# Optimization experiments

Hardware: AMD Instinct MI355X
Metric: run time of the kernel (lower is better)

Reference implementation:

```python
import jax, jax.numpy as jnp
import numpy as np

ENV_NUM = 4
# test_env = ['env1'] -> train envs are {0, 2, 3}; train pair indices i*4+j for i,j in {0,2,3}
TRAIN_INDEX = np.array([0, 2, 3, 8, 10, 11, 12, 14, 15])
CHUNK = 8  # grid points processed per step (original batch_len=4)


def setup_inputs() -> dict:
    key = jax.random.key(0)
    k1, k2 = jax.random.split(key)
    E, L, S, F = 4, 10, 1024, 256
    matrix = jax.random.normal(k1, (E, L, S, F), dtype=jnp.float32)
    # number of valid (non-padded) samples per (env, label); rest are zero-padded
    data_len = jax.random.randint(k2, (E, L), S // 2, S + 1).astype(jnp.float32)
    params = jnp.eye(F, dtype=jnp.float32)  # module initializes params = eye(feature_num)
    return {"matrix": matrix, "data_len": data_len, "params": params, "sample_size": 1024}


def _kde_forward(matrix, data_len, params, sample_size):
    E, L, S, F = matrix.shape
    bw = float(S) ** (-1.0 / 5.0)                 # max_sample ** (-1/(1+4))
    c = -0.5 / (bw * bw)                          # offset ** z == exp(c * z)
    divisor = np.sqrt(2.0 * np.pi) * bw

    m = jnp.einsum('elsf,fg->elsg', matrix, params)   # (E,L,S,F)
    # torch uses .item() for min/max -> constants w.r.t. autodiff
    left = jax.lax.stop_gradient(jnp.min(m))
    right = jax.lax.stop_gradient(jnp.max(m))
    delta = (right - left) / sample_size
    x_grid = jnp.linspace(left, right, sample_size)   # (sample_size,)

    S_f = jnp.float32(S)
    dl3 = data_len[:, :, None]                        # (E,L,1)

    def body(acc, pts):                               # pts: (CHUNK,)
        # Gaussian kernel values, (E,L,S,F,CHUNK) -- the big streamed intermediate
        z = jnp.exp(c * jnp.square(m[..., None] - pts))
        ksum = jnp.sum(z, axis=2)                     # (E,L,F,CHUNK)
        # remove contribution of the (S - data_len) zero-padded samples
        zero_corr = ((S_f - dl3) * jnp.exp(c * jnp.square(pts)))[:, :, None, :]  # (E,L,1,CHUNK)
        red = (ksum - zero_corr) / dl3[..., None]     # (E,L,F,CHUNK)
        # sum_p |red_i - red_j| over grid chunk -> (E,E,L,F)
        acc = acc + jnp.sum(jnp.abs(red[None, :] - red[:, None]), axis=-1)
        return acc, None

    n_chunks = sample_size // CHUNK
    init = jnp.zeros((E, E, L, F), dtype=matrix.dtype)
    store, _ = jax.lax.scan(body, init, x_grid.reshape(n_chunks, CHUNK))
    store_dis = store.reshape(E * E, L, F) / divisor  # divisor is constant per step

    scaled = store_dis * (delta / 2.0)
    test_results = jnp.max(scaled, axis=0)                      # (L,F)
    train_results = jnp.max(scaled[TRAIN_INDEX], axis=0)        # (L,F)
    return train_results, test_results


def reference(matrix, data_len, params, sample_size):
    return _kde_forward(matrix, data_len, params, sample_size)
```

## Files before the change

### kernel.cpp

```cpp
#include <hip/hip_runtime.h>
#include <hip/hip_fp16.h>
#include <math.h>

#define E_ 4
#define L_ 10
#define S_ 1024
#define F_ 256
#define T_ 1024
#define NROW (E_*L_*S_)
#define NBLK (NROW/64)
#define NH   48
#define CSW  224

#define OFF_PMIN 64
#define OFF_PMAX 2048
#define OFF_M   32768
#define OFF_CS  (32768 + (size_t)NROW * F_)
#define OFF_BT  (OFF_CS + (size_t)40 * F_ * CSW / 2)
#define OFF_PT  (OFF_BT + (size_t)T_ * CSW / 2)

typedef _Float16 half8 __attribute__((ext_vector_type(8)));
typedef __fp16 h2v __attribute__((ext_vector_type(2)));
typedef float f32x4v __attribute__((ext_vector_type(4)));

__device__ __forceinline__ void put_hl(_Float16* p, float v) {
  _Float16 h = (_Float16)v;
  _Float16 l = (_Float16)(v - (float)h);
  p[0] = h; p[1] = l;
}

__device__ __forceinline__ void stpk(_Float16* b, int row, int lane,
                                     float x, float y) {
  const int hi = row * 128 + ((2 * lane) ^ ((row & 7) << 3));
  *(h2v*)(b + hi) = __builtin_amdgcn_cvt_pkrtz(x, y);
}
__device__ __forceinline__ void stpk_rne(_Float16* b, int row, int lane,
                                         float x, float y) {
  const int hi = row * 128 + ((2 * lane) ^ ((row & 7) << 3));
  h2v v;
  v[0] = (__fp16)x;
  v[1] = (__fp16)y;
  *(h2v*)(b + hi) = v;
}

__global__ __launch_bounds__(256) void k_pt(const float* __restrict__ P,
                                            _Float16* __restrict__ PT) {
  const int k = blockIdx.x;
  const int c = threadIdx.x;
  PT[(size_t)c * F_ + k] = (_Float16)P[(size_t)k * F_ + c];
}

__global__ __launch_bounds__(256) void k0_mfma(const float* __restrict__ A,
                                               const _Float16* __restrict__ PT,
                                               float* __restrict__ MT,
                                               float* __restrict__ pmin,
                                               float* __restrict__ pmax) {
  __shared__ __align__(16) _Float16 Ahi[64][40];
  __shared__ __align__(16) _Float16 Alo[64][40];
  __shared__ __align__(16) _Float16 Bl[256][40];
  __shared__ float wmin[4], wmax[4];
  const int tid = threadIdx.x;
  const int wave = tid >> 6, lane = tid & 63;
  const int nn = lane & 15, quad = lane >> 4;
  const int row0 = blockIdx.x * 64;
  const int el = blockIdx.x >> 4;
  const int s0 = (blockIdx.x & 15) * 64;
  const int r = tid >> 2, part = tid & 3;
  const float* asrc = A + (size_t)(row0 + r) * F_ + part * 8;
  const _Float16* bbase = PT + (size_t)tid * F_;
  f32x4v acc[4][4];
#pragma unroll
  for (int rt = 0; rt < 4; ++rt)
#pragma unroll
    for (int ct = 0; ct < 4; ++ct) acc[rt][ct] = (f32x4v){0.f, 0.f, 0.f, 0.f};

  float4 pa0 = ((const float4*)asrc)[0];
  float4 pa1 = ((const float4*)asrc)[1];
  int4 pb0, pb1, pb2, pb3;
  {
    const int4* bs = (const int4*)bbase;
    pb0 = bs[0]; pb1 = bs[1]; pb2 = bs[2]; pb3 = bs[3];
  }

  for (int kc = 0; kc < 8; ++kc) {
    __syncthreads();
    {
      float vv[8] = {pa0.x, pa0.y, pa0.z, pa0.w, pa1.x, pa1.y, pa1.z, pa1.w};
      half8 hh, hl;
#pragma unroll
      for (int j = 0; j < 8; ++j) {
        _Float16 h = (_Float16)vv[j];
        hh[j] = h;
        hl[j] = (_Float16)(vv[j] - (float)h);
      }
      *(half8*)&Ahi[r][part * 8] = hh;
      *(half8*)&Alo[r][part * 8] = hl;
      int4* bd = (int4*)&Bl[tid][0];
      bd[0] = pb0; bd[1] = pb1; bd[2] = pb2; bd[3] = pb3;
    }
    if (kc < 7) {
      const float* an = asrc + (kc + 1) * 32;
      pa0 = ((const float4*)an)[0];
      pa1 = ((const float4*)an)[1];
      const int4* bn = (const int4*)(bbase + (kc + 1) * 32);
      pb0 = bn[0]; pb1 = bn[1]; pb2 = bn[2]; pb3 = bn[3];
    }
    __syncthreads();
    half8 afh[4], afl[4], bf[4];
#pragma unroll
    for (int rt = 0; rt < 4; ++rt) {
      afh[rt] = *(const half8*)&Ahi[rt * 16 + nn][quad * 8];
      afl[rt] = *(const half8*)&Alo[rt * 16 + nn][quad * 8];
    }
#pragma unroll
    for (int ct = 0; ct < 4; ++ct)
      bf[ct] = *(const half8*)&Bl[wave * 64 + ct * 16 + nn][quad * 8];
#pragma unroll
    for (int rt = 0; rt < 4; ++rt)
#pragma unroll
      for (int ct = 0; ct < 4; ++ct) {
        acc[rt][ct] = __builtin_amdgcn_mfma_f32_16x16x32_f16(afh[rt], bf[ct], acc[rt][ct], 0, 0, 0);
        acc[rt][ct] = __builtin_amdgcn_mfma_f32_16x16x32_f16(afl[rt], bf[ct], acc[rt][ct], 0, 0, 0);
      }
  }
  float vmin = 3.4e38f, vmax = -3.4e38f;
#pragma unroll
  for (int rt = 0; rt < 4; ++rt)
#pragma unroll
    for (int ct = 0; ct < 4; ++ct) {
      f32x4v c = acc[rt][ct];
      const int col = wave * 64 + ct * 16 + nn;
      const int sl = s0 + rt * 16 + quad * 4;
      *(float4*)&MT[((size_t)el * F_ + col) * S_ + sl] =
          make_float4(c[0], c[1], c[2], c[3]);
      vmin = fminf(vmin, fminf(fminf(c[0], c[1]), fminf(c[2], c[3])));
      vmax = fmaxf(vmax, fmaxf(fmaxf(c[0], c[1]), fmaxf(c[2], c[3])));
    }
#pragma unroll
  for (int off = 32; off; off >>= 1) {
    vmin = fminf(vmin, __shfl_down(vmin, off));
    vmax = fmaxf(vmax, __shfl_down(vmax, off));
  }
  if (lane == 0) { wmin[wave] = vmin; wmax[wave] = vmax; }
  __syncthreads();
  if (tid == 0) {
    pmin[blockIdx.x] = fminf(fminf(wmin[0], wmin[1]), fminf(wmin[2], wmin[3]));
    pmax[blockIdx.x] = fmaxf(fmaxf(wmax[0], wmax[1]), fmaxf(wmax[2], wmax[3]));
  }
}

__global__ __launch_bounds__(256) void k1_setup(const float* __restrict__ pmin,
                                                const float* __restrict__ pmax,
                                                float* __restrict__ hdr) {
  __shared__ float sm[4], sx[4];
  const int tid = threadIdx.x;
  float vmin = 3.4e38f, vmax = -3.4e38f;
  for (int i = tid; i < NBLK; i += 256) {
    vmin = fminf(vmin, pmin[i]);
    vmax = fmaxf(vmax, pmax[i]);
  }
#pragma unroll
  for (int off = 32; off; off >>= 1) {
    vmin = fminf(vmin, __shfl_down(vmin, off));
    vmax = fmaxf(vmax, __shfl_down(vmax, off));
  }
  if ((tid & 63) == 0) { sm[tid >> 6] = vmin; sx[tid >> 6] = vmax; }
  __syncthreads();
  if (tid == 0) {
    const float left = fminf(fminf(sm[0], sm[1]), fminf(sm[2], sm[3]));
    const float right = fmaxf(fmaxf(sx[0], sx[1]), fmaxf(sx[2], sx[3]));
    const float dg = (right - left) / 1023.0f;
    const float delta = (right - left) / 1024.0f;
    const float divisor = 0.62665706865775006f;
    const float scale = delta * 0.5f / divisor;
    const float Pp = (right - left) + 5.0f;
    const float sqpi8 = 0.62665706865775006f;
    hdr[0] = left; hdr[1] = dg; hdr[2] = 0.f; hdr[3] = scale;
    hdr[4] = 6.2831853071795864f / Pp;
    hdr[5] = 2.0f * sqpi8 / Pp;
    hdr[6] = sqpi8 / Pp;
  }
}

__global__ __launch_bounds__(256) void kB(const float* __restrict__ hdr,
                                          _Float16* __restrict__ BT) {
  const int t = blockIdx.x;
  const int j = threadIdx.x;
  if (j >= CSW) return;
  const float left = hdr[0], dg = hdr[1];
  const float w1 = hdr[4], asc = hdr[5], a0 = hdr[6];
  const float x = left + (float)t * dg;
  float v = 0.f;
  const int kidx = j >> 1;
  if (j < 2 * (2 * NH + 1)) {
    if (kidx == 0) v = a0;
    else if (kidx <= NH) {
      float wk = w1 * (float)kidx;
      v = asc * expf(-wk * wk * 0.03125f) * __cosf(wk * x);
    } else {
      float wk = w1 * (float)(kidx - NH);
      v = asc * expf(-wk * wk * 0.03125f) * __sinf(wk * x);
    }
  }
  BT[(size_t)t * CSW + j] = (_Float16)v;
}

__global__ __launch_bounds__(64) void kF(const float* __restrict__ MT,
                                         const float* __restrict__ hdr,
                                         _Float16* __restrict__ CS) {
  __shared__ __align__(16) _Float16 Ah[16 * 128];
  __shared__ __align__(16) _Float16 Bh[16 * 128];
  const int lane = threadIdx.x;
  const int el = blockIdx.x >> 8;
  const int f = blockIdx.x & 255;
  const float w1 = hdr[4];
  const float* src = MT + ((size_t)el * F_ + f) * S_;
  _Float16* csrow = CS + ((size_t)el * F_ + f) * CSW;

  stpk(Ah, 0, lane, 1.f, 1.f);
  stpk(Ah, 1, lane, 0.f, 0.f);
  stpk(Ah, 14, lane, 0.f, 0.f);
  stpk(Ah, 15, lane, 0.f, 0.f);
  stpk(Bh, 0, lane, 1.f, 1.f);
  stpk(Bh, 1, lane, 0.f, 0.f);

  f32x4v acc = (f32x4v){0.f, 0.f, 0.f, 0.f};
  const int rw = lane & 15, quad = lane >> 4;

  float2 nxt = ((const float2*)src)[lane];
  for (int bt = 0; bt < 8; ++bt) {
    float2 cur = nxt;
    if (bt < 7) nxt = ((const float2*)src)[(bt + 1) * 64 + lane];
    float aa = w1 * cur.x, ab = w1 * cur.y;
    float s1a, c1a, s1b, c1b;
    __sincosf(aa, &s1a, &c1a);
    __sincosf(ab, &s1b, &c1b);
    const float tca = c1a + c1a, tcb = c1b + c1b;
    stpk_rne(Bh, 2, lane, c1a, c1b);
    stpk_rne(Bh, 3, lane, s1a, s1b);
    float cpa = c1a, cppa = 1.f, spa = s1a, sppa = 0.f;
    float cpb = c1b, cppb = 1.f, spb = s1b, sppb = 0.f;
    float c2a = 0.f, c2b = 0.f, s2a = 0.f, s2b = 0.f;
#pragma unroll
    for (int rr = 2; rr <= 7; ++rr) {
      float cna = fmaf(tca, cpa, -cppa);
      float cnb = fmaf(tcb, cpb, -cppb);
      float sna = fmaf(tca, spa, -sppa);
      float snb = fmaf(tcb, spb, -sppb);
      if (rr == 2) { c2a = cna; c2b = cnb; s2a = sna; s2b = snb; }
      stpk_rne(Bh, 2 * rr, lane, cna, cnb);
      stpk_rne(Bh, 2 * rr + 1, lane, sna, snb);
      cppa = cpa; cpa = cna; cppb = cpb; cpb = cnb;
      sppa = spa; spa = sna; sppb = spb; spb = snb;
    }
    float d2a = c2a + c2a, d2b = c2b + c2b;
    float c4a = fmaf(d2a, c2a, -1.f), c4b = fmaf(d2b, c2b, -1.f);
    float s4a = d2a * s2a, s4b = d2b * s2b;
    float d4a = c4a + c4a, d4b = c4b + c4b;
    float c8a = fmaf(d4a, c4a, -1.f), c8b = fmaf(d4b, c4b, -1.f);
    float s8a = d4a * s4a, s8b = d4b * s4b;
    stpk_rne(Ah, 2, lane, c8a, c8b);
    stpk_rne(Ah, 3, lane, s8a, s8b);
    const float tqa = c8a + c8a, tqb = c8b + c8b;
    float qca = c8a, qcpa = 1.f, qsa = s8a, qspa = 0.f;
    float qcb = c8b, qcpb = 1.f, qsb = s8b, qspb = 0.f;
#pragma unroll
    for (int q = 2; q <= 6; ++q) {
      float cna = fmaf(tqa, qca, -qcpa);
      float cnb = fmaf(tqb, qcb, -qcpb);
      float sna = fmaf(tqa, qsa, -qspa);
      float snb = fmaf(tqb, qsb, -qspb);
      stpk_rne(Ah, 2 * q, lane, cna, cnb);
      stpk_rne(Ah, 2 * q + 1, lane, sna, snb);
      qcpa = qca; qca = cna; qcpb = qcb; qcb = cnb;
      qspa = qsa; qsa = sna; qspb = qsb; qsb = snb;
    }
#pragma unroll
    for (int kc = 0; kc < 4; ++kc) {
      const int off = rw * 128 + ((kc * 32 + quad * 8) ^ ((rw & 7) << 3));
      half8 af = *(const half8*)(Ah + off);
      half8 bhf = *(const half8*)(Bh + off);
      acc = __builtin_amdgcn_mfma_f32_16x16x32_f16(af, bhf, acc, 0, 0, 0);
    }
  }
  float a0 = acc[0], a1 = acc[1], a2 = acc[2], a3 = acc[3];
  float p0 = __shfl_xor(a0, 1), p1 = __shfl_xor(a1, 1);
  float p2 = __shfl_xor(a2, 1), p3 = __shfl_xor(a3, 1);
  if ((rw & 1) == 0) {
    const int rr = rw >> 1;
    const int k0v = 16 * quad + rr;
    const int k1v = 16 * quad + 8 + rr;
    float C0 = a0 - p1, S0 = a1 + p0;
    float C1 = a2 - p3, S1 = a3 + p2;
    if (k0v == 0) {
      csrow[0] = (_Float16)1024.f;
      csrow[1] = (_Float16)0.f;
    }
    if (k0v >= 1 && k0v <= NH) {
      put_hl(csrow + 2 * k0v, C0);
      put_hl(csrow + 2 * (NH + k0v), S0);
    }
    if (k1v <= NH) {
      put_hl(csrow + 2 * k1v, C1);
      put_hl(csrow + 2 * (NH + k1v), S1);
    }
  }
  if (lane < 15) {
    h2v z;
    z[0] = (__fp16)0.f;
    z[1] = (__fp16)0.f;
    *(h2v*)(csrow + 194 + 2 * lane) = z;
  }
}

__global__ __launch_bounds__(256) void kR(const _Float16* __restrict__ CS,
                                          const _Float16* __restrict__ BT,
                                          float* __restrict__ OUT) {
  const int tid = threadIdx.x;
  const int wave = tid >> 6, lane = tid & 63;
  const int nn = lane & 15, quad = lane >> 4;
  const int el = blockIdx.x >> 4;
  const int t0 = (blockIdx.x & 15) << 6;

  const _Float16* ab0 = CS + ((size_t)el * F_ + wave * 64 + 0 * 16 + nn) * CSW + quad * 8;
  const _Float16* ab1 = CS + ((size_t)el * F_ + wave * 64 + 1 * 16 + nn) * CSW + quad * 8;
  const _Float16* ab2 = CS + ((size_t)el * F_ + wave * 64 + 2 * 16 + nn) * CSW + quad * 8;
  const _Float16* ab3 = CS + ((size_t)el * F_ + wave * 64 + 3 * 16 + nn) * CSW + quad * 8;
  const _Float16* bb0 = BT + (size_t)(t0 + 0 * 16 + nn) * CSW + quad * 8;
  const _Float16* bb1 = BT + (size_t)(t0 + 1 * 16 + nn) * CSW + quad * 8;
  const _Float16* bb2 = BT + (size_t)(t0 + 2 * 16 + nn) * CSW + quad * 8;
  const _Float16* bb3 = BT + (size_t)(t0 + 3 * 16 + nn) * CSW + quad * 8;

  f32x4v acc[4][4];
#pragma unroll
  for (int ft = 0; ft < 4; ++ft)
#pragma unroll
    for (int tn = 0; tn < 4; ++tn) acc[ft][tn] = (f32x4v){0.f, 0.f, 0.f, 0.f};

  half8 pa[4], pb[4];
  pa[0] = *(const half8*)ab0; pa[1] = *(const half8*)ab1;
  pa[2] = *(const half8*)ab2; pa[3] = *(const half8*)ab3;
  pb[0] = *(const half8*)bb0; pb[1] = *(const half8*)bb1;
  pb[2] = *(const half8*)bb2; pb[3] = *(const half8*)bb3;

#pragma unroll
  for (int kc = 0; kc < CSW / 32; ++kc) {
    half8 af[4], bf[4];
#pragma unroll
    for (int ft = 0; ft < 4; ++ft) af[ft] = pa[ft];
#pragma unroll
    for (int tn = 0; tn < 4; ++tn) bf[tn] = pb[tn];
    if (kc < CSW / 32 - 1) {
      const int o = (kc + 1) * 32;
      pa[0] = *(const half8*)(ab0 + o); pa[1] = *(const half8*)(ab1 + o);
      pa[2] = *(const half8*)(ab2 + o); pa[3] = *(const half8*)(ab3 + o);
      pb[0] = *(const half8*)(bb0 + o); pb[1] = *(const half8*)(bb1 + o);
      pb[2] = *(const half8*)(bb2 + o); pb[3] = *(const half8*)(bb3 + o);
    }
#pragma unroll
    for (int ft = 0; ft < 4; ++ft)
#pragma unroll
      for (int tn = 0; tn < 4; ++tn)
        acc[ft][tn] = __builtin_amdgcn_mfma_f32_16x16x32_f16(af[ft], bf[tn], acc[ft][tn], 0, 0, 0);
  }

  float* Ob = OUT + (size_t)el * F_ * T_ + t0;
#pragma unroll
  for (int ft = 0; ft < 4; ++ft)
#pragma unroll
    for (int tn = 0; tn < 4; ++tn) {
      f32x4v c = acc[ft][tn];
      const int fb = wave * 64 + ft * 16 + quad * 4;
      const int tc = tn * 16 + nn;
      Ob[(size_t)(fb + 0) * T_ + tc] = c[0];
      Ob[(size_t)(fb + 1) * T_ + tc] = c[1];
      Ob[(size_t)(fb + 2) * T_ + tc] = c[2];
      Ob[(size_t)(fb + 3) * T_ + tc] = c[3];
    }
}

__global__ __launch_bounds__(256) void k4_epi(const float* __restrict__ OUT,
                                              const float* __restrict__ hdr,
                                              const float* __restrict__ dl,
                                              float* __restrict__ out) {
  __shared__ float rs[4][6];
  const int tid = threadIdx.x;
  const int l = blockIdx.x >> 8;
  const int f = blockIdx.x & 255;
  const float left = hdr[0], dg = hdr[1], scale = hdr[3];
  const int t = 4 * tid;
  float etv[4];
#pragma unroll
  for (int d = 0; d < 4; ++d) {
    float x = left + (float)(t + d) * dg;
    etv[d] = expf(-8.0f * x * x);
  }
  float red[E_][4];
#pragma unroll
  for (int e = 0; e < E_; ++e) {
    float4 ks = *(const float4*)(OUT + (((size_t)(e * L_ + l)) * F_ + f) * T_ + t);
    const float dlv = dl[e * L_ + l];
    const float zc = (float)S_ - dlv;
    const float idl = 1.0f / dlv;
    red[e][0] = (ks.x - zc * etv[0]) * idl;
    red[e][1] = (ks.y - zc * etv[1]) * idl;
    red[e][2] = (ks.z - zc * etv[2]) * idl;
    red[e][3] = (ks.w - zc * etv[3]) * idl;
  }
  float D[6];
  const int pa[6] = {0, 0, 0, 1, 1, 2};
  const int pb[6] = {1, 2, 3, 2, 3, 3};
#pragma unroll
  for (int p = 0; p < 6; ++p) {
    float s = 0.f;
#pragma unroll
    for (int d = 0; d < 4; ++d) s += fabsf(red[pa[p]][d] - red[pb[p]][d]);
    D[p] = s;
  }
#pragma unroll
  for (int off = 32; off; off >>= 1)
#pragma unroll
    for (int p = 0; p < 6; ++p) D[p] += __shfl_down(D[p], off);
  if ((tid & 63) == 0) {
#pragma unroll
    for (int p = 0; p < 6; ++p) rs[tid >> 6][p] = D[p];
  }
  __syncthreads();
  if (tid == 0) {
    float Tp[6];
#pragma unroll
    for (int p = 0; p < 6; ++p)
      Tp[p] = (rs[0][p] + rs[1][p] + rs[2][p] + rs[3][p]) * scale;
    float test = Tp[0];
#pragma unroll
    for (int p = 1; p < 6; ++p) test = fmaxf(test, Tp[p]);
    float train = fmaxf(fmaxf(Tp[1], Tp[2]), Tp[5]);
    out[l * F_ + f] = train;
    out[L_ * F_ + l * F_ + f] = test;
  }
}

extern "C" void kernel_launch(void* const* d_in, const int* in_sizes, int n_in,
                              void* d_out, int out_size, void* d_ws, size_t ws_size,
                              hipStream_t stream) {
  const float* A  = (const float*)d_in[0];
  const float* dl = (const float*)d_in[1];
  const float* P  = (const float*)d_in[2];
  float* out = (float*)d_out;
  float* ws = (float*)d_ws;
  float* hdr = ws;
  float* pmin = ws + OFF_PMIN;
  float* pmax = ws + OFF_PMAX;
  float* MT  = ws + OFF_M;
  float* OUT = ws + OFF_M;
  _Float16* CS = (_Float16*)(ws + OFF_CS);
  _Float16* BT = (_Float16*)(ws + OFF_BT);
  _Float16* PT = (_Float16*)(ws + OFF_PT);

  k_pt<<<F_, 256, 0, stream>>>(P, PT);
  k0_mfma<<<NBLK, 256, 0, stream>>>(A, PT, MT, pmin, pmax);
  k1_setup<<<1, 256, 0, stream>>>(pmin, pmax, hdr);
  kB<<<T_, 256, 0, stream>>>(hdr, BT);
  kF<<<E_ * L_ * F_, 64, 0, stream>>>(MT, hdr, CS);
  kR<<<(E_ * L_) * 16, 256, 0, stream>>>(CS, BT, OUT);
  k4_epi<<<L_ * F_, 256, 0, stream>>>(OUT, hdr, dl, out);
}
```

Baseline: 160.9 us.

## Fuse setup, basis-table and Fourier kernels into one launch with per-wave range reduction

Removes the single-block setup kernel. Each wave now recomputes the global min/max itself from the per-block partials (640 entries), both in the new combined kernel and in the epilogue. The basis-table generation and the per-feature Fourier-coefficient kernel are merged into one launch via block-index dispatch. The Fourier part now packs four 64-thread waves per 256-thread block with per-wave shared buffers. This saves two kernel launches and their serialization gaps, at the cost of redundant reads of the partial min/max arrays in every wave.

```diff
diff --git a/kernel.cpp b/kernel.cpp
--- a/kernel.cpp
+++ b/kernel.cpp
@@ -27,6 +27,23 @@
   _Float16 h = (_Float16)v;
   _Float16 l = (_Float16)(v - (float)h);
   p[0] = h; p[1] = l;
+}
+
+__device__ __forceinline__ void wave_range(const float* __restrict__ pmin,
+                                           const float* __restrict__ pmax,
+                                           float& left, float& right) {
+  const int lane = threadIdx.x & 63;
+  float vmin = 3.4e38f, vmax = -3.4e38f;
+  for (int i = lane; i < NBLK; i += 64) {
+    vmin = fminf(vmin, pmin[i]);
+    vmax = fmaxf(vmax, pmax[i]);
+  }
+#pragma unroll
+  for (int off = 32; off; off >>= 1) {
+    vmin = fminf(vmin, __shfl_xor(vmin, off));
+    vmax = fmaxf(vmax, __shfl_xor(vmax, off));
+  }
+  left = vmin; right = vmax;
 }
 
 __device__ __forceinline__ void stpk(_Float16* b, int row, int lane,
@@ -149,73 +166,52 @@
   }
 }
 
-__global__ __launch_bounds__(256) void k1_setup(const float* __restrict__ pmin,
-                                                const float* __restrict__ pmax,
-                                                float* __restrict__ hdr) {
-  __shared__ float sm[4], sx[4];
-  const int tid = threadIdx.x;
-  float vmin = 3.4e38f, vmax = -3.4e38f;
-  for (int i = tid; i < NBLK; i += 256) {
-    vmin = fminf(vmin, pmin[i]);
-    vmax = fmaxf(vmax, pmax[i]);
-  }
-#pragma unroll
-  for (int off = 32; off; off >>= 1) {
-    vmin = fminf(vmin, __shfl_down(vmin, off));
-    vmax = fmaxf(vmax, __shfl_down(vmax, off));
-  }
-  if ((tid & 63) == 0) { sm[tid >> 6] = vmin; sx[tid >> 6] = vmax; }
-  __syncthreads();
-  if (tid == 0) {
-    const float left = fminf(fminf(sm[0], sm[1]), fminf(sm[2], sm[3]));
-    const float right = fmaxf(fmaxf(sx[0], sx[1]), fmaxf(sx[2], sx[3]));
+__global__ __launch_bounds__(256) void kBF(const float* __restrict__ pmin,
+                                           const float* __restrict__ pmax,
+                                           _Float16* __restrict__ BT,
+                                           const float* __restrict__ MT,
+                                           _Float16* __restrict__ CS) {
+  __shared__ __align__(16) _Float16 AhS[4][16 * 128];
+  __shared__ __align__(16) _Float16 BhS[4][16 * 128];
+  float left, right;
+  wave_range(pmin, pmax, left, right);
+  const float Pp = (right - left) + 5.0f;
+  const float w1 = 6.2831853071795864f / Pp;
+
+  if (blockIdx.x < T_) {
+    const int t = blockIdx.x;
+    const int j = threadIdx.x;
+    if (j >= CSW) return;
     const float dg = (right - left) / 1023.0f;
-    const float delta = (right - left) / 1024.0f;
-    const float divisor = 0.62665706865775006f;
-    const float scale = delta * 0.5f / divisor;
-    const float Pp = (right - left) + 5.0f;
     const float sqpi8 = 0.62665706865775006f;
-    hdr[0] = left; hdr[1] = dg; hdr[2] = 0.f; hdr[3] = scale;
-    hdr[4] = 6.2831853071795864f / Pp;
-    hdr[5] = 2.0f * sqpi8 / Pp;
-    hdr[6] = sqpi8 / Pp;
-  }
-}
-
-__global__ __launch_bounds__(256) void kB(const float* __restrict__ hdr,
-                                          _Float16* __restrict__ BT) {
-  const int t = blockIdx.x;
-  const int j = threadIdx.x;
-  if (j >= CSW) return;
-  const float left = hdr[0], dg = hdr[1];
-  const float w1 = hdr[4], asc = hdr[5], a0 = hdr[6];
-  const float x = left + (float)t * dg;
-  float v = 0.f;
-  const int kidx = j >> 1;
-  if (j < 2 * (2 * NH + 1)) {
-    if (kidx == 0) v = a0;
-    else if (kidx <= NH) {
-      float wk = w1 * (float)kidx;
-      v = asc * expf(-wk * wk * 0.03125f) * __cosf(wk * x);
-    } else {
-      float wk = w1 * (float)(kidx - NH);
-      v = asc * expf(-wk * wk * 0.03125f) * __sinf(wk * x);
-    }
-  }
-  BT[(size_t)t * CSW + j] = (_Float16)v;
-}
-
-__global__ __launch_bounds__(64) void kF(const float* __restrict__ MT,
-                                         const float* __restrict__ hdr,
-                                         _Float16* __restrict__ CS) {
-  __shared__ __align__(16) _Float16 Ah[16 * 128];
-  __shared__ __align__(16) _Float16 Bh[16 * 128];
-  const int lane = threadIdx.x;
-  const int el = blockIdx.x >> 8;
-  const int f = blockIdx.x & 255;
-  const float w1 = hdr[4];
+    const float asc = 2.0f * sqpi8 / Pp;
+    const float a0 = sqpi8 / Pp;
+    const float x = left + (float)t * dg;
+    float v = 0.f;
+    const int kidx = j >> 1;
+    if (j < 2 * (2 * NH + 1)) {
+      if (kidx == 0) v = a0;
+      else if (kidx <= NH) {
+        float wk = w1 * (float)kidx;
+        v = asc * expf(-wk * wk * 0.03125f) * __cosf(wk * x);
+      } else {
+        float wk = w1 * (float)(kidx - NH);
+        v = asc * expf(-wk * wk * 0.03125f) * __sinf(wk * x);
+      }
+    }
+    BT[(size_t)t * CSW + j] = (_Float16)v;
+    return;
+  }
+
+  const int wave = threadIdx.x >> 6;
+  const int lane = threadIdx.x & 63;
+  const int fi = (blockIdx.x - T_) * 4 + wave;
+  const int el = fi >> 8;
+  const int f = fi & 255;
   const float* src = MT + ((size_t)el * F_ + f) * S_;
   _Float16* csrow = CS + ((size_t)el * F_ + f) * CSW;
+  _Float16* Ah = AhS[wave];
+  _Float16* Bh = BhS[wave];
 
   stpk(Ah, 0, lane, 1.f, 1.f);
   stpk(Ah, 1, lane, 0.f, 0.f);
@@ -283,15 +279,15 @@
       acc = __builtin_amdgcn_mfma_f32_16x16x32_f16(af, bhf, acc, 0, 0, 0);
     }
   }
-  float a0 = acc[0], a1 = acc[1], a2 = acc[2], a3 = acc[3];
-  float p0 = __shfl_xor(a0, 1), p1 = __shfl_xor(a1, 1);
-  float p2 = __shfl_xor(a2, 1), p3 = __shfl_xor(a3, 1);
+  float a0v = acc[0], a1v = acc[1], a2v = acc[2], a3v = acc[3];
+  float p0 = __shfl_xor(a0v, 1), p1 = __shfl_xor(a1v, 1);
+  float p2 = __shfl_xor(a2v, 1), p3 = __shfl_xor(a3v, 1);
   if ((rw & 1) == 0) {
     const int rr = rw >> 1;
     const int k0v = 16 * quad + rr;
     const int k1v = 16 * quad + 8 + rr;
-    float C0 = a0 - p1, S0 = a1 + p0;
-    float C1 = a2 - p3, S1 = a3 + p2;
+    float C0 = a0v - p1, S0 = a1v + p0;
+    float C1 = a2v - p3, S1 = a3v + p2;
     if (k0v == 0) {
       csrow[0] = (_Float16)1024.f;
       csrow[1] = (_Float16)0.f;
@@ -380,14 +376,19 @@
 }
 
 __global__ __launch_bounds__(256) void k4_epi(const float* __restrict__ OUT,
-                                              const float* __restrict__ hdr,
+                                              const float* __restrict__ pmin,
+                                              const float* __restrict__ pmax,
                                               const float* __restrict__ dl,
                                               float* __restrict__ out) {
   __shared__ float rs[4][6];
   const int tid = threadIdx.x;
   const int l = blockIdx.x >> 8;
   const int f = blockIdx.x & 255;
-  const float left = hdr[0], dg = hdr[1], scale = hdr[3];
+  float left, right;
+  wave_range(pmin, pmax, left, right);
+  const float dg = (right - left) / 1023.0f;
+  const float delta = (right - left) / 1024.0f;
+  const float scale = delta * 0.5f / 0.62665706865775006f;
   const int t = 4 * tid;
   float etv[4];
 #pragma unroll
@@ -448,7 +449,6 @@
   const float* P  = (const float*)d_in[2];
   float* out = (float*)d_out;
   float* ws = (float*)d_ws;
-  float* hdr = ws;
   float* pmin = ws + OFF_PMIN;
   float* pmax = ws + OFF_PMAX;
   float* MT  = ws + OFF_M;
@@ -459,9 +459,7 @@
 
   k_pt<<<F_, 256, 0, stream>>>(P, PT);
   k0_mfma<<<NBLK, 256, 0, stream>>>(A, PT, MT, pmin, pmax);
-  k1_setup<<<1, 256, 0, stream>>>(pmin, pmax, hdr);
-  kB<<<T_, 256, 0, stream>>>(hdr, BT);
-  kF<<<E_ * L_ * F_, 64, 0, stream>>>(MT, hdr, CS);
+  kBF<<<T_ + (E_ * L_ * F_) / 4, 256, 0, stream>>>(pmin, pmax, BT, MT, CS);
   kR<<<(E_ * L_) * 16, 256, 0, stream>>>(CS, BT, OUT);
-  k4_epi<<<L_ * F_, 256, 0, stream>>>(OUT, hdr, dl, out);
-}
+  k4_epi<<<L_ * F_, 256, 0, stream>>>(OUT, pmin, pmax, dl, out);
+}
```

Result: slower. 165.9 us (+3.1%).
